# Kernel optimization log

Hardware: AMD Instinct MI355X
Metric: run time of the kernel (lower is better)

## Reference

```python
import jax, jax.numpy as jnp
import numpy as np

INPUT_SIZE = 512
OUTPUT_CLASS = 2
BATCH, INST_NUM = 4, 40000


def setup_inputs() -> dict:
    key = jax.random.key(0)
    ks = jax.random.split(key, 8)
    s_in = 1.0 / np.sqrt(INPUT_SIZE)
    s_h = 1.0 / np.sqrt(128)
    return {
        "feats": jax.random.normal(ks[0], (BATCH, INST_NUM, INPUT_SIZE), jnp.float32),
        "c": jax.random.normal(ks[1], (BATCH, INST_NUM, OUTPUT_CLASS), jnp.float32),
        "q_w1": jax.random.uniform(ks[2], (INPUT_SIZE, 128), jnp.float32, -s_in, s_in),
        "q_b1": jax.random.uniform(ks[3], (128,), jnp.float32, -s_in, s_in),
        "q_w2": jax.random.uniform(ks[4], (128, 128), jnp.float32, -s_h, s_h),
        "q_b2": jax.random.uniform(ks[5], (128,), jnp.float32, -s_h, s_h),
        "fcc_w": jax.random.uniform(ks[6], (OUTPUT_CLASS, OUTPUT_CLASS, INPUT_SIZE), jnp.float32, -s_in, s_in),
        "fcc_b": jax.random.uniform(ks[7], (OUTPUT_CLASS,), jnp.float32, -s_in, s_in),
    }


def _q_mlp(x, w1, b1, w2, b2):
    h = jax.nn.relu(x @ w1 + b1)
    return jnp.tanh(h @ w2 + b2)


def reference(feats, c, q_w1, q_b1, q_w2, q_b2, fcc_w, fcc_b):
    batch, inst_num, dim = feats.shape
    V = feats  # passing_v=False -> Identity
    Q = _q_mlp(feats, q_w1, q_b1, q_w2, q_b2)  # [b, n, 128]
    # top instance per class: sort descending, take first -> argmax along instances
    top_idx = jnp.argmax(c, axis=1)  # [b, output_class]
    m_feats = jnp.take_along_axis(feats, top_idx[:, :, None], axis=1)  # [b, oc, dim]
    q_max = _q_mlp(m_feats, q_w1, q_b1, q_w2, q_b2)  # [b, oc, 128]
    # NOTE: original divides by sqrt(Q.shape[1]) == sqrt(inst_num)
    scale = jnp.sqrt(jnp.float32(inst_num))
    A = jnp.einsum('bnk,bok->bno', Q, q_max) / scale  # [b, n, oc]
    A = jax.nn.softmax(A, axis=1)  # softmax over instances
    B = jnp.einsum('bno,bnd->bod', A, V)  # [b, oc, dim]
    # Conv1d(oc, oc, kernel=dim) on B -> full contraction over (in_ch, dim)
    C = jnp.einsum('bid,oid->bo', B, fcc_w) + fcc_b  # [b, oc]
    return C, A, B
```

## Files before the change

kernel.cpp:

```cpp
#include <hip/hip_runtime.h>
#include <hip/hip_bf16.h>

#define NB 4
#define NI 40000
#define DI 512
#define NH 128
#define TM 32
#define NTB 1250
#define SPB 64

typedef __attribute__((ext_vector_type(8))) short bf16x8;
typedef __attribute__((ext_vector_type(4))) float f32x4;

#define GLOAD_LDS16(gp, lp)                                                     \
    __builtin_amdgcn_global_load_lds(                                           \
        (const __attribute__((address_space(1))) void*)(gp),                    \
        (__attribute__((address_space(3))) void*)(lp), 16, 0, 0)

#define ASM_VMCNT8() asm volatile("s_waitcnt vmcnt(8)" ::: "memory")
#define ASM_VMCNT0() asm volatile("s_waitcnt vmcnt(0)" ::: "memory")
#define ASM_LGKM0()  asm volatile("s_waitcnt lgkmcnt(0)" ::: "memory")
#define SCHED0()     __builtin_amdgcn_sched_barrier(0)
#define SBAR()       { asm volatile("" ::: "memory"); __builtin_amdgcn_s_barrier(); asm volatile("" ::: "memory"); }

__device__ __forceinline__ ushort f2b(float f) {
    union { float f; unsigned u; } x; x.f = f;
    unsigned r = x.u + 0x7FFFu + ((x.u >> 16) & 1u);
    return (ushort)(r >> 16);
}
__device__ __forceinline__ float tanh_fast(float x) {
    x = fminf(15.f, fmaxf(-15.f, x));
    float e = __expf(2.f * x);
    return (e - 1.f) / (e + 1.f);
}

__global__ void k_wt(const float* __restrict__ w1, const float* __restrict__ w2,
                     ushort* __restrict__ w1t, ushort* __restrict__ w2t) {
    int idx = blockIdx.x * 256 + threadIdx.x;
    if (idx < 65536) {
        int j = idx >> 9, i = idx & 511;
        w1t[idx] = f2b(w1[i * 128 + j]);
    } else if (idx < 81920) {
        int r = idx - 65536;
        int j = r >> 7, k = r & 127;
        w2t[r] = f2b(w2[k * 128 + j]);
    }
}

__global__ void k_am1(const float* __restrict__ c, float* __restrict__ pv, int* __restrict__ pi) {
    int blk = blockIdx.x;
    int bo = blk >> 4, ch = blk & 15;
    int b = bo >> 1, o = bo & 1;
    __shared__ float rv[256];
    __shared__ int   ri[256];
    int tid = threadIdx.x;
    float bv = -3.402823466e38f; int bi = 0x7fffffff;
    for (int n = ch * 2500 + tid; n < (ch + 1) * 2500; n += 256) {
        float v = c[((size_t)b * NI + n) * 2 + o];
        if (v > bv || (v == bv && n < bi)) { bv = v; bi = n; }
    }
    rv[tid] = bv; ri[tid] = bi;
    __syncthreads();
    for (int s = 128; s > 0; s >>= 1) {
        if (tid < s) {
            if (rv[tid + s] > rv[tid] || (rv[tid + s] == rv[tid] && ri[tid + s] < ri[tid])) {
                rv[tid] = rv[tid + s]; ri[tid] = ri[tid + s];
            }
        }
        __syncthreads();
    }
    if (tid == 0) { pv[blk] = rv[0]; pi[blk] = ri[0]; }
}

__global__ void k_am2(const float* __restrict__ pv, const int* __restrict__ pi,
                      int* __restrict__ topidx) {
    int bo = blockIdx.x;
    if (threadIdx.x == 0) {
        float bv = -3.402823466e38f; int bi = 0x7fffffff;
        for (int ch = 0; ch < 16; ++ch) {
            float v = pv[bo * 16 + ch]; int idx = pi[bo * 16 + ch];
            if (v > bv || (v == bv && idx < bi)) { bv = v; bi = idx; }
        }
        topidx[bo] = bi;
    }
}

__global__ void k_qmax(const float* __restrict__ feats, const int* __restrict__ topidx,
                       const float* __restrict__ w1, const float* __restrict__ b1,
                       const float* __restrict__ w2, const float* __restrict__ b2,
                       float* __restrict__ qmax) {
    int bo = blockIdx.x;
    int b = bo >> 1;
    __shared__ float xs[DI];
    __shared__ float hs[NH];
    int tid = threadIdx.x;
    const float* x = feats + ((size_t)b * NI + topidx[bo]) * DI;
    if (tid < DI) xs[tid] = x[tid];
    __syncthreads();
    int j = tid >> 2, part = tid & 3;
    float p = 0.f;
    for (int i = part * 128; i < part * 128 + 128; ++i)
        p += xs[i] * w1[i * NH + j];
    p += __shfl_xor(p, 1); p += __shfl_xor(p, 2);
    if (part == 0) { float h = p + b1[j]; hs[j] = h > 0.f ? h : 0.f; }
    __syncthreads();
    p = 0.f;
    for (int i = part * 32; i < part * 32 + 32; ++i)
        p += hs[i] * w2[i * NH + j];
    p += __shfl_xor(p, 1); p += __shfl_xor(p, 2);
    if (part == 0) qmax[bo * NH + j] = tanhf(p + b2[j]);
}

__global__ __launch_bounds__(512, 2)
void k_main(const float* __restrict__ feats,
            const ushort* __restrict__ w1t, const ushort* __restrict__ w2t,
            const float* __restrict__ b1, const float* __restrict__ b2,
            const float* __restrict__ qmax,
            float* __restrict__ ews, float* __restrict__ zp, float* __restrict__ Up) {
    __shared__ __align__(16) char x_lds[2 * 65536];
    __shared__ ushort h_lds[TM * NH];
    __shared__ float  sp_lds[4][TM][2];
    __shared__ float  e_lds[TM * 2];

    const int tid  = threadIdx.x;
    const int wave = tid >> 6;
    const int lane = tid & 63;
    const int sub  = blockIdx.x & (SPB - 1);
    const int b    = blockIdx.x >> 6;

    const int wm = wave >> 2;
    const int wn = wave & 3;
    const int lr = lane & 15;
    const int lk = (lane >> 4) * 8;
    const int l4 = (lane >> 4) * 4;

    const int col0 = wn * 32 + lr;
    const int col1 = col0 + 16;
    const float rb1_0 = b1[col0], rb1_1 = b1[col1];
    const float rb2_0 = b2[col0], rb2_1 = b2[col1];
    const float qm00 = qmax[b * 256 + col0];
    const float qm01 = qmax[b * 256 + col1];
    const float qm10 = qmax[b * 256 + NH + col0];
    const float qm11 = qmax[b * 256 + NH + col1];

    bf16x8 W1f0[16], W1f1[16];
    {
        const ushort* wc0 = w1t + (size_t)col0 * DI + lk;
        const ushort* wc1 = w1t + (size_t)col1 * DI + lk;
#pragma unroll
        for (int ks = 0; ks < 16; ++ks) {
            W1f0[ks] = *(const bf16x8*)(wc0 + ks * 32);
            W1f1[ks] = *(const bf16x8*)(wc1 + ks * 32);
        }
    }
    bf16x8 W2f0[4], W2f1[4];
#pragma unroll
    for (int ks = 0; ks < 4; ++ks) {
        W2f0[ks] = *(const bf16x8*)&w2t[(size_t)col0 * NH + ks * 32 + lk];
        W2f1[ks] = *(const bf16x8*)&w2t[(size_t)col1 * NH + ks * 32 + lk];
    }

    const int cnt = (NTB - sub + SPB - 1) / SPB;
    const float* fb = feats + (size_t)b * NI * DI;

    float u0 = 0.f, u1 = 0.f, zacc = 0.f;

    auto issue_tile = [&](int i, int bufsel) {
        const char* xg = (const char*)(fb + (size_t)(sub + SPB * i) * TM * DI);
        char* lbase = x_lds + bufsel * 65536 + wave * 1024;
#pragma unroll
        for (int q = 0; q < 8; ++q) {
            int idx = q * 512 + tid;
            int row = idx >> 7, c4 = idx & 127;
            const char* src = xg + row * 2048 + ((c4 ^ (row & 7)) << 4);
            GLOAD_LDS16(src, lbase + q * 8192);
        }
    };

    issue_tile(0, 0);
    issue_tile(1, 1);
    ASM_VMCNT8();
    SCHED0();
    SBAR();

    int cur = 0;
    for (int i = 0; i < cnt; ++i) {
        const int n0 = (sub + SPB * i) * TM;
        const char* bufc = x_lds + cur * 65536;

        f32x4 acc0 = {}, acc1 = {};
        {
            const char* arow = bufc + (wm * 16 + lr) * 2048;
            const int rsw = lr & 7;
#pragma unroll
            for (int ks = 0; ks < 16; ++ks) {
                int c4a = ks * 8 + (lk >> 2);
                float4 xa = *(const float4*)(arow + ((c4a ^ rsw) << 4));
                float4 xb = *(const float4*)(arow + (((c4a + 1) ^ rsw) << 4));
                unsigned p0, p1, p2, p3;
                asm("v_cvt_pk_bf16_f32 %0, %1, %2" : "=v"(p0) : "v"(xa.x), "v"(xa.y));
                asm("v_cvt_pk_bf16_f32 %0, %1, %2" : "=v"(p1) : "v"(xa.z), "v"(xa.w));
                asm("v_cvt_pk_bf16_f32 %0, %1, %2" : "=v"(p2) : "v"(xb.x), "v"(xb.y));
                asm("v_cvt_pk_bf16_f32 %0, %1, %2" : "=v"(p3) : "v"(xb.z), "v"(xb.w));
                union { unsigned u[4]; bf16x8 v; } af;
                af.u[0] = p0; af.u[1] = p1; af.u[2] = p2; af.u[3] = p3;
                acc0 = __builtin_amdgcn_mfma_f32_16x16x32_bf16(af.v, W1f0[ks], acc0, 0, 0, 0);
                acc1 = __builtin_amdgcn_mfma_f32_16x16x32_bf16(af.v, W1f1[ks], acc1, 0, 0, 0);
            }
        }

#pragma unroll
        for (int r = 0; r < 4; ++r) {
            int row = wm * 16 + l4 + r;
            float v0 = acc0[r] + rb1_0;
            float v1 = acc1[r] + rb1_1;
            *(ushort*)((char*)h_lds + row * 256 + ((col0 * 2) ^ ((row & 7) << 4))) =
                f2b(v0 > 0.f ? v0 : 0.f);
            *(ushort*)((char*)h_lds + row * 256 + ((col1 * 2) ^ ((row & 7) << 4))) =
                f2b(v1 > 0.f ? v1 : 0.f);
        }
        ASM_LGKM0();
        SBAR();

        f32x4 c20 = {}, c21 = {};
        {
            const char* hrow = (const char*)h_lds + (wm * 16 + lr) * 256;
            const int rsw2 = (lr & 7) << 4;
#pragma unroll
            for (int ks = 0; ks < 4; ++ks) {
                bf16x8 a = *(const bf16x8*)(hrow + ((ks * 64 + lk * 2) ^ rsw2));
                c20 = __builtin_amdgcn_mfma_f32_16x16x32_bf16(a, W2f0[ks], c20, 0, 0, 0);
                c21 = __builtin_amdgcn_mfma_f32_16x16x32_bf16(a, W2f1[ks], c21, 0, 0, 0);
            }
        }

#pragma unroll
        for (int r = 0; r < 4; ++r) {
            float q0 = tanh_fast(c20[r] + rb2_0);
            float q1 = tanh_fast(c21[r] + rb2_1);
            float p0 = q0 * qm00 + q1 * qm01;
            float p1 = q0 * qm10 + q1 * qm11;
            p0 += __shfl_xor(p0, 1); p1 += __shfl_xor(p1, 1);
            p0 += __shfl_xor(p0, 2); p1 += __shfl_xor(p1, 2);
            p0 += __shfl_xor(p0, 4); p1 += __shfl_xor(p1, 4);
            p0 += __shfl_xor(p0, 8); p1 += __shfl_xor(p1, 8);
            if (lr == 0) {
                int row = wm * 16 + l4 + r;
                sp_lds[wn][row][0] = p0;
                sp_lds[wn][row][1] = p1;
            }
        }
        ASM_LGKM0();
        SBAR();

        if (tid < 64) {
            int row = tid >> 1, o = tid & 1;
            float s = (sp_lds[0][row][o] + sp_lds[1][row][o] +
                       sp_lds[2][row][o] + sp_lds[3][row][o]) * 0.005f;
            float e = __expf(s);
            e_lds[row * 2 + o] = e;
            ews[((size_t)(b * NI + n0 + row)) * 2 + o] = e;
            float z = e;
            z += __shfl_xor(z, 2);  z += __shfl_xor(z, 4);
            z += __shfl_xor(z, 8);  z += __shfl_xor(z, 16);
            z += __shfl_xor(z, 32);
            if (tid < 2) zacc += z;
        }
        ASM_LGKM0();
        SBAR();

        {
            int slot = tid >> 2, lo4 = (tid & 3) * 4;
#pragma unroll 8
            for (int n = 0; n < TM; ++n) {
                float x = *(const float*)(bufc + n * 2048 + ((slot ^ (n & 7)) << 4) + lo4);
                u0 += e_lds[n * 2] * x;
                u1 += e_lds[n * 2 + 1] * x;
            }
        }
        ASM_LGKM0();
        SBAR();

        if (i + 2 < cnt) {
            issue_tile(i + 2, cur);
            ASM_VMCNT8();
        } else {
            ASM_VMCNT0();
        }
        SCHED0();
        SBAR();
        cur ^= 1;
    }

    {
        size_t base = ((size_t)(b * SPB + sub) * 2) * DI;
        Up[base + tid] = u0;
        Up[base + DI + tid] = u1;
        if (tid < 2) zp[(b * SPB + sub) * 2 + tid] = zacc;
    }
}

__global__ void k_zred(const float* __restrict__ zp, float* __restrict__ Zt) {
    int bo = blockIdx.x; int b = bo >> 1, o = bo & 1;
    int tid = threadIdx.x;
    float z = zp[(b * SPB + tid) * 2 + o];
    z += __shfl_xor(z, 1);  z += __shfl_xor(z, 2);
    z += __shfl_xor(z, 4);  z += __shfl_xor(z, 8);
    z += __shfl_xor(z, 16); z += __shfl_xor(z, 32);
    if (tid == 0) Zt[bo] = z;
}

__global__ void k_A(const float* __restrict__ ews, const float* __restrict__ Zt,
                    float* __restrict__ outA) {
    int idx = blockIdx.x * 256 + threadIdx.x;
    int b = idx / (NI * 2);
    int o = idx & 1;
    outA[idx] = ews[idx] / Zt[b * 2 + o];
}

__global__ void k_B(const float* __restrict__ Up, const float* __restrict__ Zt,
                    float* __restrict__ outB) {
    int bo = blockIdx.x; int d = threadIdx.x;
    int b = bo >> 1, o = bo & 1;
    float u = 0.f;
    for (int s2 = 0; s2 < SPB; ++s2)
        u += Up[(((size_t)(b * SPB + s2)) * 2 + o) * DI + d];
    outB[bo * DI + d] = u / Zt[bo];
}

__global__ void k_C(const float* __restrict__ outB, const float* __restrict__ fcc_w,
                    const float* __restrict__ fcc_b, float* __restrict__ outC) {
    int bo = blockIdx.x; int b = bo >> 1, o = bo & 1;
    __shared__ float red[256];
    int tid = threadIdx.x;
    float acc = 0.f;
    for (int idx = tid; idx < 2 * DI; idx += 256) {
        int i = idx >> 9, d = idx & 511;
        acc += outB[(b * 2 + i) * DI + d] * fcc_w[o * (2 * DI) + i * DI + d];
    }
    red[tid] = acc; __syncthreads();
    for (int s = 128; s > 0; s >>= 1) {
        if (tid < s) red[tid] += red[tid + s];
        __syncthreads();
    }
    if (tid == 0) outC[bo] = red[0] + fcc_b[o];
}

extern "C" void kernel_launch(void* const* d_in, const int* in_sizes, int n_in,
                              void* d_out, int out_size, void* d_ws, size_t ws_size,
                              hipStream_t stream) {
    const float* feats = (const float*)d_in[0];
    const float* c     = (const float*)d_in[1];
    const float* q_w1  = (const float*)d_in[2];
    const float* q_b1  = (const float*)d_in[3];
    const float* q_w2  = (const float*)d_in[4];
    const float* q_b2  = (const float*)d_in[5];
    const float* fcc_w = (const float*)d_in[6];
    const float* fcc_b = (const float*)d_in[7];
    float* out = (float*)d_out;

    char* w = (char*)d_ws;
    ushort* w1t  = (ushort*)(w);
    ushort* w2t  = (ushort*)(w + 131072);
    float* qmaxb = (float*)(w + 163840);
    int*   topi  = (int*)(w + 167936);
    float* Zt    = (float*)(w + 167968);
    float* pv    = (float*)(w + 168000);
    int*   pi    = (int*)(w + 168512);
    float* ews   = (float*)(w + 169024);
    float* zp    = (float*)(w + 1449024);
    float* Up    = (float*)(w + 1451072);

    float* outC = out;
    float* outA = out + 8;
    float* outB = out + 8 + NB * NI * 2;

    k_wt<<<320, 256, 0, stream>>>(q_w1, q_w2, w1t, w2t);
    k_am1<<<128, 256, 0, stream>>>(c, pv, pi);
    k_am2<<<8, 64, 0, stream>>>(pv, pi, topi);
    k_qmax<<<8, 512, 0, stream>>>(feats, topi, q_w1, q_b1, q_w2, q_b2, qmaxb);
    k_main<<<NB * SPB, 512, 0, stream>>>(feats, w1t, w2t, q_b1, q_b2, qmaxb, ews, zp, Up);
    k_zred<<<8, 64, 0, stream>>>(zp, Zt);
    k_A<<<NB * NI * 2 / 256, 256, 0, stream>>>(ews, Zt, outA);
    k_B<<<8, 512, 0, stream>>>(Up, Zt, outB);
    k_C<<<8, 256, 0, stream>>>(outB, fcc_w, fcc_b, outC);
}
```

Before: 217.1 us.

## Stage feature tiles as bf16 via register prefetch and double the block count

Result: slower. 280.0 us (+29.0%).

```diff
diff --git a/kernel.cpp b/kernel.cpp
--- a/kernel.cpp
+++ b/kernel.cpp
@@ -7,26 +7,22 @@
 #define NH 128
 #define TM 32
 #define NTB 1250
-#define SPB 64
+#define SPB 128
 
 typedef __attribute__((ext_vector_type(8))) short bf16x8;
 typedef __attribute__((ext_vector_type(4))) float f32x4;
 
-#define GLOAD_LDS16(gp, lp)                                                     \
-    __builtin_amdgcn_global_load_lds(                                           \
-        (const __attribute__((address_space(1))) void*)(gp),                    \
-        (__attribute__((address_space(3))) void*)(lp), 16, 0, 0)
-
-#define ASM_VMCNT8() asm volatile("s_waitcnt vmcnt(8)" ::: "memory")
-#define ASM_VMCNT0() asm volatile("s_waitcnt vmcnt(0)" ::: "memory")
 #define ASM_LGKM0()  asm volatile("s_waitcnt lgkmcnt(0)" ::: "memory")
-#define SCHED0()     __builtin_amdgcn_sched_barrier(0)
 #define SBAR()       { asm volatile("" ::: "memory"); __builtin_amdgcn_s_barrier(); asm volatile("" ::: "memory"); }
 
 __device__ __forceinline__ ushort f2b(float f) {
     union { float f; unsigned u; } x; x.f = f;
     unsigned r = x.u + 0x7FFFu + ((x.u >> 16) & 1u);
     return (ushort)(r >> 16);
+}
+__device__ __forceinline__ float b2f(ushort u) {
+    union { unsigned u; float f; } x; x.u = ((unsigned)u) << 16;
+    return x.f;
 }
 __device__ __forceinline__ float tanh_fast(float x) {
     x = fminf(15.f, fmaxf(-15.f, x));
@@ -111,28 +107,28 @@
     if (part == 0) qmax[bo * NH + j] = tanhf(p + b2[j]);
 }
 
-__global__ __launch_bounds__(512, 2)
+__global__ __launch_bounds__(256, 2)
 void k_main(const float* __restrict__ feats,
             const ushort* __restrict__ w1t, const ushort* __restrict__ w2t,
             const float* __restrict__ b1, const float* __restrict__ b2,
             const float* __restrict__ qmax,
             float* __restrict__ ews, float* __restrict__ zp, float* __restrict__ Up) {
-    __shared__ __align__(16) char x_lds[2 * 65536];
+    __shared__ __align__(16) char x_lds[2 * 32768];
     __shared__ ushort h_lds[TM * NH];
     __shared__ float  sp_lds[4][TM][2];
     __shared__ float  e_lds[TM * 2];
 
     const int tid  = threadIdx.x;
-    const int wave = tid >> 6;
+    const int wn   = tid >> 6;
     const int lane = tid & 63;
     const int sub  = blockIdx.x & (SPB - 1);
-    const int b    = blockIdx.x >> 6;
-
-    const int wm = wave >> 2;
-    const int wn = wave & 3;
-    const int lr = lane & 15;
-    const int lk = (lane >> 4) * 8;
-    const int l4 = (lane >> 4) * 4;
+    const int b    = blockIdx.x >> 7;
+
+    const int lr  = lane & 15;
+    const int lkg = lane >> 4;
+    const int lk  = lkg * 8;
+    const int l4  = lkg * 4;
+    const int rsw = lr & 7;
 
     const int col0 = wn * 32 + lr;
     const int col1 = col0 + 16;
@@ -143,113 +139,137 @@
     const float qm10 = qmax[b * 256 + NH + col0];
     const float qm11 = qmax[b * 256 + NH + col1];
 
-    bf16x8 W1f0[16], W1f1[16];
-    {
-        const ushort* wc0 = w1t + (size_t)col0 * DI + lk;
-        const ushort* wc1 = w1t + (size_t)col1 * DI + lk;
-#pragma unroll
-        for (int ks = 0; ks < 16; ++ks) {
-            W1f0[ks] = *(const bf16x8*)(wc0 + ks * 32);
-            W1f1[ks] = *(const bf16x8*)(wc1 + ks * 32);
-        }
-    }
     bf16x8 W2f0[4], W2f1[4];
 #pragma unroll
     for (int ks = 0; ks < 4; ++ks) {
         W2f0[ks] = *(const bf16x8*)&w2t[(size_t)col0 * NH + ks * 32 + lk];
         W2f1[ks] = *(const bf16x8*)&w2t[(size_t)col1 * NH + ks * 32 + lk];
     }
+    const ushort* wb0 = w1t + (size_t)col0 * DI + lk;
+    const ushort* wb1 = w1t + (size_t)col1 * DI + lk;
 
     const int cnt = (NTB - sub + SPB - 1) / SPB;
     const float* fb = feats + (size_t)b * NI * DI;
 
-    float u0 = 0.f, u1 = 0.f, zacc = 0.f;
-
-    auto issue_tile = [&](int i, int bufsel) {
-        const char* xg = (const char*)(fb + (size_t)(sub + SPB * i) * TM * DI);
-        char* lbase = x_lds + bufsel * 65536 + wave * 1024;
-#pragma unroll
-        for (int q = 0; q < 8; ++q) {
-            int idx = q * 512 + tid;
+    float u00 = 0.f, u01 = 0.f, u10 = 0.f, u11 = 0.f, zacc = 0.f;
+
+    float4 pf[16];
+
+    auto issue_loads = [&](int i) {
+        const float4* xg4 = (const float4*)(fb + (size_t)(sub + SPB * i) * TM * DI);
+#pragma unroll
+        for (int q = 0; q < 16; ++q) pf[q] = xg4[tid + q * 256];
+    };
+    auto write_tile = [&](int bufsel) {
+        char* xb = x_lds + bufsel * 32768;
+#pragma unroll
+        for (int q = 0; q < 16; ++q) {
+            int idx = tid + q * 256;
             int row = idx >> 7, c4 = idx & 127;
-            const char* src = xg + row * 2048 + ((c4 ^ (row & 7)) << 4);
-            GLOAD_LDS16(src, lbase + q * 8192);
+            unsigned lo, hi;
+            asm("v_cvt_pk_bf16_f32 %0, %1, %2" : "=v"(lo) : "v"(pf[q].x), "v"(pf[q].y));
+            asm("v_cvt_pk_bf16_f32 %0, %1, %2" : "=v"(hi) : "v"(pf[q].z), "v"(pf[q].w));
+            uint2 u; u.x = lo; u.y = hi;
+            *(uint2*)(xb + row * 1024 + ((((c4 >> 1) ^ (row & 7)) << 4) | ((c4 & 1) * 8))) = u;
         }
     };
 
-    issue_tile(0, 0);
-    issue_tile(1, 1);
-    ASM_VMCNT8();
-    SCHED0();
+    issue_loads(0);
+    write_tile(0);
+    if (1 < cnt) issue_loads(1);
+    ASM_LGKM0();
     SBAR();
 
     int cur = 0;
     for (int i = 0; i < cnt; ++i) {
         const int n0 = (sub + SPB * i) * TM;
-        const char* bufc = x_lds + cur * 65536;
-
-        f32x4 acc0 = {}, acc1 = {};
+        const char* xb = x_lds + cur * 32768;
+        const char* xr0 = xb + lr * 1024;
+        const char* xr1 = xb + (16 + lr) * 1024;
+
+        f32x4 acc00 = {}, acc01 = {}, acc10 = {}, acc11 = {};
         {
-            const char* arow = bufc + (wm * 16 + lr) * 2048;
-            const int rsw = lr & 7;
-#pragma unroll
-            for (int ks = 0; ks < 16; ++ks) {
-                int c4a = ks * 8 + (lk >> 2);
-                float4 xa = *(const float4*)(arow + ((c4a ^ rsw) << 4));
-                float4 xb = *(const float4*)(arow + (((c4a + 1) ^ rsw) << 4));
-                unsigned p0, p1, p2, p3;
-                asm("v_cvt_pk_bf16_f32 %0, %1, %2" : "=v"(p0) : "v"(xa.x), "v"(xa.y));
-                asm("v_cvt_pk_bf16_f32 %0, %1, %2" : "=v"(p1) : "v"(xa.z), "v"(xa.w));
-                asm("v_cvt_pk_bf16_f32 %0, %1, %2" : "=v"(p2) : "v"(xb.x), "v"(xb.y));
-                asm("v_cvt_pk_bf16_f32 %0, %1, %2" : "=v"(p3) : "v"(xb.z), "v"(xb.w));
-                union { unsigned u[4]; bf16x8 v; } af;
-                af.u[0] = p0; af.u[1] = p1; af.u[2] = p2; af.u[3] = p3;
-                acc0 = __builtin_amdgcn_mfma_f32_16x16x32_bf16(af.v, W1f0[ks], acc0, 0, 0, 0);
-                acc1 = __builtin_amdgcn_mfma_f32_16x16x32_bf16(af.v, W1f1[ks], acc1, 0, 0, 0);
+            bf16x8 WA0[4], WA1[4], WB0[4], WB1[4];
+#pragma unroll
+            for (int j = 0; j < 4; ++j) {
+                WA0[j] = *(const bf16x8*)(wb0 + j * 32);
+                WA1[j] = *(const bf16x8*)(wb1 + j * 32);
+            }
+#pragma unroll
+            for (int g = 0; g < 4; ++g) {
+                bf16x8* C0 = (g & 1) ? WB0 : WA0;
+                bf16x8* C1 = (g & 1) ? WB1 : WA1;
+                bf16x8* N0 = (g & 1) ? WA0 : WB0;
+                bf16x8* N1 = (g & 1) ? WA1 : WB1;
+                if (g < 3) {
+#pragma unroll
+                    for (int j = 0; j < 4; ++j) {
+                        N0[j] = *(const bf16x8*)(wb0 + (g + 1) * 128 + j * 32);
+                        N1[j] = *(const bf16x8*)(wb1 + (g + 1) * 128 + j * 32);
+                    }
+                }
+#pragma unroll
+                for (int j = 0; j < 4; ++j) {
+                    int ks = g * 4 + j;
+                    int off = ((ks * 4 + lkg) ^ rsw) << 4;
+                    bf16x8 a0 = *(const bf16x8*)(xr0 + off);
+                    bf16x8 a1 = *(const bf16x8*)(xr1 + off);
+                    acc00 = __builtin_amdgcn_mfma_f32_16x16x32_bf16(a0, C0[j], acc00, 0, 0, 0);
+                    acc01 = __builtin_amdgcn_mfma_f32_16x16x32_bf16(a0, C1[j], acc01, 0, 0, 0);
+                    acc10 = __builtin_amdgcn_mfma_f32_16x16x32_bf16(a1, C0[j], acc10, 0, 0, 0);
+                    acc11 = __builtin_amdgcn_mfma_f32_16x16x32_bf16(a1, C1[j], acc11, 0, 0, 0);
+                }
             }
         }
 
 #pragma unroll
         for (int r = 0; r < 4; ++r) {
-            int row = wm * 16 + l4 + r;
-            float v0 = acc0[r] + rb1_0;
-            float v1 = acc1[r] + rb1_1;
-            *(ushort*)((char*)h_lds + row * 256 + ((col0 * 2) ^ ((row & 7) << 4))) =
-                f2b(v0 > 0.f ? v0 : 0.f);
-            *(ushort*)((char*)h_lds + row * 256 + ((col1 * 2) ^ ((row & 7) << 4))) =
-                f2b(v1 > 0.f ? v1 : 0.f);
+            int row0 = l4 + r, row1 = 16 + l4 + r;
+            float v00 = acc00[r] + rb1_0, v01 = acc01[r] + rb1_1;
+            float v10 = acc10[r] + rb1_0, v11 = acc11[r] + rb1_1;
+            *(ushort*)((char*)h_lds + row0 * 256 + ((col0 * 2) ^ ((row0 & 7) << 4))) = f2b(v00 > 0.f ? v00 : 0.f);
+            *(ushort*)((char*)h_lds + row0 * 256 + ((col1 * 2) ^ ((row0 & 7) << 4))) = f2b(v01 > 0.f ? v01 : 0.f);
+            *(ushort*)((char*)h_lds + row1 * 256 + ((col0 * 2) ^ ((row1 & 7) << 4))) = f2b(v10 > 0.f ? v10 : 0.f);
+            *(ushort*)((char*)h_lds + row1 * 256 + ((col1 * 2) ^ ((row1 & 7) << 4))) = f2b(v11 > 0.f ? v11 : 0.f);
         }
         ASM_LGKM0();
         SBAR();
 
-        f32x4 c20 = {}, c21 = {};
+        f32x4 c200 = {}, c201 = {}, c210 = {}, c211 = {};
         {
-            const char* hrow = (const char*)h_lds + (wm * 16 + lr) * 256;
-            const int rsw2 = (lr & 7) << 4;
+            const char* hr0 = (const char*)h_lds + lr * 256;
+            const char* hr1 = (const char*)h_lds + (16 + lr) * 256;
+            const int rsw2 = rsw << 4;
 #pragma unroll
             for (int ks = 0; ks < 4; ++ks) {
-                bf16x8 a = *(const bf16x8*)(hrow + ((ks * 64 + lk * 2) ^ rsw2));
-                c20 = __builtin_amdgcn_mfma_f32_16x16x32_bf16(a, W2f0[ks], c20, 0, 0, 0);
-                c21 = __builtin_amdgcn_mfma_f32_16x16x32_bf16(a, W2f1[ks], c21, 0, 0, 0);
-            }
-        }
-
-#pragma unroll
-        for (int r = 0; r < 4; ++r) {
-            float q0 = tanh_fast(c20[r] + rb2_0);
-            float q1 = tanh_fast(c21[r] + rb2_1);
-            float p0 = q0 * qm00 + q1 * qm01;
-            float p1 = q0 * qm10 + q1 * qm11;
-            p0 += __shfl_xor(p0, 1); p1 += __shfl_xor(p1, 1);
-            p0 += __shfl_xor(p0, 2); p1 += __shfl_xor(p1, 2);
-            p0 += __shfl_xor(p0, 4); p1 += __shfl_xor(p1, 4);
-            p0 += __shfl_xor(p0, 8); p1 += __shfl_xor(p1, 8);
-            if (lr == 0) {
-                int row = wm * 16 + l4 + r;
-                sp_lds[wn][row][0] = p0;
-                sp_lds[wn][row][1] = p1;
-            }
-        }
+                int off = (ks * 64 + lk * 2) ^ rsw2;
+                bf16x8 a0 = *(const bf16x8*)(hr0 + off);
+                bf16x8 a1 = *(const bf16x8*)(hr1 + off);
+                c200 = __builtin_amdgcn_mfma_f32_16x16x32_bf16(a0, W2f0[ks], c200, 0, 0, 0);
+                c201 = __builtin_amdgcn_mfma_f32_16x16x32_bf16(a0, W2f1[ks], c201, 0, 0, 0);
+                c210 = __builtin_amdgcn_mfma_f32_16x16x32_bf16(a1, W2f0[ks], c210, 0, 0, 0);
+                c211 = __builtin_amdgcn_mfma_f32_16x16x32_bf16(a1, W2f1[ks], c211, 0, 0, 0);
+            }
+        }
+
+#pragma unroll
+        for (int m = 0; m < 2; ++m)
+#pragma unroll
+            for (int r = 0; r < 4; ++r) {
+                float q0 = tanh_fast((m ? c210[r] : c200[r]) + rb2_0);
+                float q1 = tanh_fast((m ? c211[r] : c201[r]) + rb2_1);
+                float p0 = q0 * qm00 + q1 * qm01;
+                float p1 = q0 * qm10 + q1 * qm11;
+                p0 += __shfl_xor(p0, 1); p1 += __shfl_xor(p1, 1);
+                p0 += __shfl_xor(p0, 2); p1 += __shfl_xor(p1, 2);
+                p0 += __shfl_xor(p0, 4); p1 += __shfl_xor(p1, 4);
+                p0 += __shfl_xor(p0, 8); p1 += __shfl_xor(p1, 8);
+                if (lr == 0) {
+                    int row = m * 16 + l4 + r;
+                    sp_lds[wn][row][0] = p0;
+                    sp_lds[wn][row][1] = p1;
+                }
+            }
         ASM_LGKM0();
         SBAR();
 
@@ -269,33 +289,32 @@
         ASM_LGKM0();
         SBAR();
 
+        if (i + 1 < cnt) write_tile(cur ^ 1);
+        if (i + 2 < cnt) issue_loads(i + 2);
+
         {
-            int slot = tid >> 2, lo4 = (tid & 3) * 4;
+            const int gsl = tid >> 2, lo4 = (tid & 3) * 4;
 #pragma unroll 8
             for (int n = 0; n < TM; ++n) {
-                float x = *(const float*)(bufc + n * 2048 + ((slot ^ (n & 7)) << 4) + lo4);
-                u0 += e_lds[n * 2] * x;
-                u1 += e_lds[n * 2 + 1] * x;
+                unsigned v = *(const unsigned*)(xb + n * 1024 + (((gsl ^ (n & 7)) << 4) | lo4));
+                float2 ev = *(const float2*)&e_lds[n * 2];
+                float x0 = b2f((ushort)(v & 0xffff));
+                float x1 = b2f((ushort)(v >> 16));
+                u00 += ev.x * x0; u01 += ev.x * x1;
+                u10 += ev.y * x0; u11 += ev.y * x1;
             }
         }
         ASM_LGKM0();
         SBAR();
-
-        if (i + 2 < cnt) {
-            issue_tile(i + 2, cur);
-            ASM_VMCNT8();
-        } else {
-            ASM_VMCNT0();
-        }
-        SCHED0();
-        SBAR();
         cur ^= 1;
     }
 
     {
         size_t base = ((size_t)(b * SPB + sub) * 2) * DI;
-        Up[base + tid] = u0;
-        Up[base + DI + tid] = u1;
+        float2 v0; v0.x = u00; v0.y = u01;
+        float2 v1; v1.x = u10; v1.y = u11;
+        *(float2*)&Up[base + tid * 2] = v0;
+        *(float2*)&Up[base + DI + tid * 2] = v1;
         if (tid < 2) zp[(b * SPB + sub) * 2 + tid] = zacc;
     }
 }
@@ -303,7 +322,7 @@
 __global__ void k_zred(const float* __restrict__ zp, float* __restrict__ Zt) {
     int bo = blockIdx.x; int b = bo >> 1, o = bo & 1;
     int tid = threadIdx.x;
-    float z = zp[(b * SPB + tid) * 2 + o];
+    float z = zp[(b * SPB + tid) * 2 + o] + zp[(b * SPB + tid + 64) * 2 + o];
     z += __shfl_xor(z, 1);  z += __shfl_xor(z, 2);
     z += __shfl_xor(z, 4);  z += __shfl_xor(z, 8);
     z += __shfl_xor(z, 16); z += __shfl_xor(z, 32);
@@ -369,7 +388,7 @@
     int*   pi    = (int*)(w + 168512);
     float* ews   = (float*)(w + 169024);
     float* zp    = (float*)(w + 1449024);
-    float* Up    = (float*)(w + 1451072);
+    float* Up    = (float*)(w + 1453120);
 
     float* outC = out;
     float* outA = out + 8;
@@ -379,7 +398,7 @@
     k_am1<<<128, 256, 0, stream>>>(c, pv, pi);
     k_am2<<<8, 64, 0, stream>>>(pv, pi, topi);
     k_qmax<<<8, 512, 0, stream>>>(feats, topi, q_w1, q_b1, q_w2, q_b2, qmaxb);
-    k_main<<<NB * SPB, 512, 0, stream>>>(feats, w1t, w2t, q_b1, q_b2, qmaxb, ews, zp, Up);
+    k_main<<<NB * SPB, 256, 0, stream>>>(feats, w1t, w2t, q_b1, q_b2, qmaxb, ews, zp, Up);
     k_zred<<<8, 64, 0, stream>>>(zp, Zt);
     k_A<<<NB * NI * 2 / 256, 256, 0, stream>>>(ews, Zt, outA);
     k_B<<<8, 512, 0, stream>>>(Up, Zt, outB);
```
